# Kernel tuning notes

Hardware: AMD Instinct MI355X
Metric: run time of the kernel (lower is better)

Reference implementation:

```python
import jax, jax.numpy as jnp
import numpy as np

NUM_GROUPS = 32
EPS = 1e-6


def group_norm(x, w, b):
    # x: (B, C, L); normalize per group of C//32 channels over (channels-in-group, L)
    B, C, L = x.shape
    xg = x.reshape(B, NUM_GROUPS, C // NUM_GROUPS, L)
    mean = jnp.mean(xg, axis=(2, 3), keepdims=True)
    var = jnp.var(xg, axis=(2, 3), keepdims=True)
    xn = ((xg - mean) * jax.lax.rsqrt(var + EPS)).reshape(B, C, L)
    return xn * w[None, :, None] + b[None, :, None]


def conv1x1(x, w, b):
    # 1x1 Conv1d == channel-mixing linear. x: (B,C,L), w: (O,C), b: (O,)
    return jnp.einsum('oc,bcl->bol', w, x) + b[None, :, None]


def setup_inputs() -> dict:
    key = jax.random.key(0)
    ks = jax.random.split(key, 6)
    B, C, L = 8, 512, 2048
    s = 1.0 / np.sqrt(C)
    return {
        'x': jax.random.normal(ks[0], (B, C, L), dtype=jnp.float32),
        'gn_w': jnp.ones((C,), jnp.float32),
        'gn_b': jnp.zeros((C,), jnp.float32),
        'wq': jax.random.normal(ks[1], (C, C), dtype=jnp.float32) * s,
        'bq': jnp.zeros((C,), jnp.float32),
        'wk': jax.random.normal(ks[2], (C, C), dtype=jnp.float32) * s,
        'bk': jnp.zeros((C,), jnp.float32),
        'wv': jax.random.normal(ks[3], (C, C), dtype=jnp.float32) * s,
        'bv': jnp.zeros((C,), jnp.float32),
        'wo': jax.random.normal(ks[4], (C, C), dtype=jnp.float32) * s,
        'bo': jnp.zeros((C,), jnp.float32),
    }


def reference(x, gn_w, gn_b, wq, bq, wk, bk, wv, bv, wo, bo):
    B, C, L = x.shape
    h = group_norm(x, gn_w, gn_b)
    q = conv1x1(h, wq, bq)  # (B,C,L)
    k = conv1x1(h, wk, bk)
    v = conv1x1(h, wv, bv)
    scale = jnp.asarray(C, x.dtype) ** -0.5
    # scores over length: w[b,i,j] = sum_c q[b,c,i] k[b,c,j]
    w_ = jnp.einsum('bci,bcj->bij', q, k) * scale
    w_ = jax.nn.softmax(w_, axis=-1)
    # h[b,c,i] = sum_j w[b,i,j] v[b,c,j]
    h = jnp.einsum('bij,bcj->bci', w_, v)
    h = conv1x1(h, wo, bo)
    return x + h
```

## Files before the change

### kernel.cpp

```cpp
#include <hip/hip_runtime.h>
#include <math.h>

#define BATCH 8
#define CH 512
#define LEN 2048
#define NG 32
#define CPG 16

typedef unsigned short u16;
typedef __bf16 bf16x8 __attribute__((ext_vector_type(8)));
typedef float f32x16 __attribute__((ext_vector_type(16)));

__device__ __forceinline__ u16 f2bf(float f) {
    union { float f; unsigned u; } c; c.f = f;
    unsigned r = c.u + 0x7fffu + ((c.u >> 16) & 1u);
    return (u16)(r >> 16);
}
__device__ __forceinline__ float bf2f(u16 h) {
    union { unsigned u; float f; } c; c.u = ((unsigned)h) << 16;
    return c.f;
}
__device__ __forceinline__ void gload16(const u16* g, u16* l) {
    __builtin_amdgcn_global_load_lds(
        (const __attribute__((address_space(1))) unsigned int*)g,
        (__attribute__((address_space(3))) unsigned int*)l, 16, 0, 0);
}

__global__ __launch_bounds__(256) void fused_pre(
    const float* __restrict__ x,
    const float* __restrict__ w0, const float* __restrict__ w1,
    const float* __restrict__ w2, const float* __restrict__ w3,
    u16* __restrict__ o0, u16* __restrict__ o1,
    u16* __restrict__ o2, u16* __restrict__ o3,
    float4* __restrict__ zbuf, float* __restrict__ stats) {
    const int blk = blockIdx.x;
    if (blk < 16) {
        zbuf[blk * 256 + threadIdx.x] = make_float4(0.f, 0.f, 0.f, 0.f);
    } else if (blk < 1040) {
        const int wb = blk - 16;
        const float* s; u16* d;
        switch (wb >> 8) {
            case 0: s = w0; d = o0; break;
            case 1: s = w1; d = o1; break;
            case 2: s = w2; d = o2; break;
            default: s = w3; d = o3; break;
        }
        const int i = (wb & 255) * 256 + threadIdx.x;
        float4 f = ((const float4*)s)[i];
        ((ushort4*)d)[i] = make_ushort4(f2bf(f.x), f2bf(f.y), f2bf(f.z), f2bf(f.w));
    } else {
        const int sb = blk - 1040;
        const int b = sb >> 7, g = (sb >> 2) & 31, sl = sb & 3;
        const float4* xp = (const float4*)(x + ((size_t)b * CH + (size_t)g * CPG) * LEN) + sl * 2048;
        float s = 0.f, s2 = 0.f;
        #pragma unroll
        for (int i = 0; i < 8; ++i) {
            float4 v = xp[threadIdx.x + i * 256];
            s += v.x + v.y + v.z + v.w;
            s2 = fmaf(v.x, v.x, fmaf(v.y, v.y, fmaf(v.z, v.z, fmaf(v.w, v.w, s2))));
        }
        #pragma unroll
        for (int off = 32; off > 0; off >>= 1) {
            s  += __shfl_down(s, off, 64);
            s2 += __shfl_down(s2, off, 64);
        }
        __shared__ float sm[2][4];
        const int lane = threadIdx.x & 63, wv = threadIdx.x >> 6;
        if (lane == 0) { sm[0][wv] = s; sm[1][wv] = s2; }
        __syncthreads();
        if (threadIdx.x == 0) {
            const int base = (b * NG + g) * 4 + sl;
            stats[base]        = sm[0][0] + sm[0][1] + sm[0][2] + sm[0][3];
            stats[1024 + base] = sm[1][0] + sm[1][1] + sm[1][2] + sm[1][3];
        }
    }
}

__global__ __launch_bounds__(256) void gn_apply_t(const float* __restrict__ x,
                                                  const float* __restrict__ stats,
                                                  const float* __restrict__ gw,
                                                  const float* __restrict__ gb,
                                                  u16* __restrict__ Ht) {
    __shared__ float tile[64][65];
    const int b = blockIdx.z, c0 = blockIdx.y * 64, l0 = blockIdx.x * 64;
    const int t = threadIdx.x;
    const int rid = t >> 4, q = t & 15;
    const float inv = 1.f / (CPG * LEN);
    #pragma unroll
    for (int pass = 0; pass < 4; ++pass) {
        const int c = rid + pass * 16;
        const int ca = c0 + c;
        const int base = (b * NG + (ca >> 4)) * 4;
        const float S  = stats[base + 0] + stats[base + 1] + stats[base + 2] + stats[base + 3];
        const float S2 = stats[1024 + base + 0] + stats[1024 + base + 1]
                       + stats[1024 + base + 2] + stats[1024 + base + 3];
        const float mean = S * inv;
        const float var  = S2 * inv - mean * mean;
        const float a  = rsqrtf(var + 1e-6f) * gw[ca];
        const float sh = gb[ca] - mean * a;
        const float4 v = *(const float4*)&x[((size_t)b * CH + ca) * LEN + l0 + q * 4];
        tile[c][q * 4 + 0] = v.x * a + sh;
        tile[c][q * 4 + 1] = v.y * a + sh;
        tile[c][q * 4 + 2] = v.z * a + sh;
        tile[c][q * 4 + 3] = v.w * a + sh;
    }
    __syncthreads();
    #pragma unroll
    for (int pass = 0; pass < 4; ++pass) {
        const int l = rid + pass * 16;
        ushort4 o;
        o.x = f2bf(tile[q * 4 + 0][l]);
        o.y = f2bf(tile[q * 4 + 1][l]);
        o.z = f2bf(tile[q * 4 + 2][l]);
        o.w = f2bf(tile[q * 4 + 3][l]);
        *(ushort4*)&Ht[((size_t)b * LEN + l0 + l) * CH + c0 + q * 4] = o;
    }
}

#define EPI_QK   0
#define EPI_TBN  1
#define EPI_EXP  2
#define EPI_TNRM 3
#define EPI_FIN  4

template <int MODE>
__global__ __launch_bounds__(256, 4) void gemm_bt(
    const u16* __restrict__ A, int lda, long long sA,
    const u16* __restrict__ B, int ldb, long long sB,
    void* __restrict__ Out, void* __restrict__ Out2,
    int ldo, long long sO,
    const float* __restrict__ bias, const float* __restrict__ bias2,
    const float* __restrict__ res, long long sR,
    float* __restrict__ rsum, long long sRS,
    int K, float alpha) {
    __shared__ u16 As[128 * 64];
    __shared__ u16 Bs[128 * 64];

    int bz, by, bx;
    if (MODE == EPI_EXP) {
        const int gx = gridDim.x, gy = gridDim.y;
        int flat = (blockIdx.z * gy + blockIdx.y) * gx + blockIdx.x;
        const int nbk = gx * gy * (int)gridDim.z;
        flat = (flat & 7) * (nbk >> 3) + (flat >> 3);
        bz = flat / (gx * gy);
        const int rr = flat - bz * gx * gy;
        by = rr / gx;
        bx = rr - by * gx;
    } else {
        bz = blockIdx.z; by = blockIdx.y; bx = blockIdx.x;
    }

    const int n0 = bx * 128, m0 = by * 128;
    A += (size_t)bz * sA;
    B += (size_t)bz * sB;
    const int t = threadIdx.x;
    const int lane = t & 63, wid = t >> 6;

    const int rowL = t >> 3, kq = (t & 7) ^ (rowL & 7);
    unsigned aoff = (unsigned)((m0 + rowL) * lda + kq * 8);
    unsigned boff = (unsigned)((n0 + rowL) * ldb + kq * 8);
    u16* const lds_dst_a = As + t * 8;
    u16* const lds_dst_b = Bs + t * 8;

    f32x16 acc[2][2];
    #pragma unroll
    for (int i = 0; i < 2; ++i)
        #pragma unroll
        for (int j = 0; j < 2; ++j)
            acc[i][j] = (f32x16)(0.f);

    const int col = lane & 31, half = lane >> 5;
    const int wm = (wid & 1) * 64, wn = (wid >> 1) * 64;
    const int mf = wm + col, nf = wn + col;
    const int mswz = mf & 7, nswz = nf & 7;

    for (int k0 = 0; k0 < K; k0 += 64) {
        #pragma unroll
        for (int g = 0; g < 4; ++g) {
            gload16(A + aoff + g * (32 * lda), lds_dst_a + g * 2048);
            gload16(B + boff + g * (32 * ldb), lds_dst_b + g * 2048);
        }
        aoff += 64; boff += 64;
        __syncthreads();
        #pragma unroll
        for (int ks = 0; ks < 4; ++ks) {
            const int kcA = ((ks * 2 + half) ^ mswz) * 8;
            const int kcB = ((ks * 2 + half) ^ nswz) * 8;
            bf16x8 a0 = *(const bf16x8*)(As + (mf)      * 64 + kcA);
            bf16x8 a1 = *(const bf16x8*)(As + (mf + 32) * 64 + kcA);
            bf16x8 b0 = *(const bf16x8*)(Bs + (nf)      * 64 + kcB);
            bf16x8 b1 = *(const bf16x8*)(Bs + (nf + 32) * 64 + kcB);
            acc[0][0] = __builtin_amdgcn_mfma_f32_32x32x16_bf16(a0, b0, acc[0][0], 0, 0, 0);
            acc[0][1] = __builtin_amdgcn_mfma_f32_32x32x16_bf16(a0, b1, acc[0][1], 0, 0, 0);
            acc[1][0] = __builtin_amdgcn_mfma_f32_32x32x16_bf16(a1, b0, acc[1][0], 0, 0, 0);
            acc[1][1] = __builtin_amdgcn_mfma_f32_32x32x16_bf16(a1, b1, acc[1][1], 0, 0, 0);
        }
        __syncthreads();
    }

    if (MODE == EPI_FIN) {
        float* O = (float*)Out + (size_t)bz * sO;
        const float* R = res + (size_t)bz * sR;
        #pragma unroll
        for (int im = 0; im < 2; ++im)
            #pragma unroll
            for (int g4 = 0; g4 < 4; ++g4) {
                const int mb = m0 + wm + im * 32 + g4 * 8 + half * 4;
                #pragma unroll
                for (int jn = 0; jn < 2; ++jn) {
                    const int n = n0 + wn + jn * 32 + col;
                    const float bb = bias[n];
                    const size_t base = (size_t)n * ldo + mb;
                    const float4 r4 = *(const float4*)&R[base];
                    float4 o4;
                    o4.x = acc[im][jn][g4 * 4 + 0] + bb + r4.x;
                    o4.y = acc[im][jn][g4 * 4 + 1] + bb + r4.y;
                    o4.z = acc[im][jn][g4 * 4 + 2] + bb + r4.z;
                    o4.w = acc[im][jn][g4 * 4 + 3] + bb + r4.w;
                    *(float4*)&O[base] = o4;
                }
            }
    } else if (MODE == EPI_EXP) {
        u16* O = (u16*)Out + (size_t)bz * sO;
        float* RS = rsum + (size_t)bz * sRS;
        float psum[2] = {0.f, 0.f};
        #pragma unroll
        for (int im = 0; im < 2; ++im)
            #pragma unroll
            for (int g4 = 0; g4 < 4; ++g4) {
                const int mb = m0 + wm + im * 32 + g4 * 8 + half * 4;
                #pragma unroll
                for (int jn = 0; jn < 2; ++jn) {
                    const int n = n0 + wn + jn * 32 + col;
                    u16 h0 = f2bf(__expf(acc[im][jn][g4 * 4 + 0] * alpha));
                    u16 h1 = f2bf(__expf(acc[im][jn][g4 * 4 + 1] * alpha));
                    u16 h2 = f2bf(__expf(acc[im][jn][g4 * 4 + 2] * alpha));
                    u16 h3 = f2bf(__expf(acc[im][jn][g4 * 4 + 3] * alpha));
                    psum[jn] += bf2f(h0) + bf2f(h1) + bf2f(h2) + bf2f(h3);
                    *(ushort4*)&O[(size_t)n * ldo + mb] = make_ushort4(h0, h1, h2, h3);
                }
            }
        #pragma unroll
        for (int jn = 0; jn < 2; ++jn) psum[jn] += __shfl_xor(psum[jn], 32, 64);
        if (half == 0) {
            #pragma unroll
            for (int jn = 0; jn < 2; ++jn)
                atomicAdd(&RS[n0 + wn + jn * 32 + col], psum[jn]);
        }
    } else {
        u16* O;
        const float* bi = bias;
        const float* RS = (MODE == EPI_TNRM) ? rsum + (size_t)bz * sRS : nullptr;
        int mbase = m0 + wm;
        if (MODE == EPI_QK) {
            const bool hi = (m0 & 512) != 0;
            O  = (u16*)(hi ? Out2 : Out) + (size_t)bz * sO;
            bi = hi ? bias2 : bias;
            mbase = (m0 & 511) + wm;
        } else {
            O = (u16*)Out + (size_t)bz * sO;
        }
        float inv[2];
        if (MODE == EPI_TNRM) {
            inv[0] = 1.f / RS[n0 + wn + col];
            inv[1] = 1.f / RS[n0 + wn + 32 + col];
        }
        #pragma unroll
        for (int im = 0; im < 2; ++im)
            #pragma unroll
            for (int g4 = 0; g4 < 4; ++g4) {
                const int mb = mbase + im * 32 + g4 * 8 + half * 4;
                float4 bm = make_float4(0.f, 0.f, 0.f, 0.f);
                if (MODE == EPI_QK) bm = *(const float4*)&bi[mb];
                #pragma unroll
                for (int jn = 0; jn < 2; ++jn) {
                    const int n = n0 + wn + jn * 32 + col;
                    float v0 = acc[im][jn][g4 * 4 + 0];
                    float v1 = acc[im][jn][g4 * 4 + 1];
                    float v2 = acc[im][jn][g4 * 4 + 2];
                    float v3 = acc[im][jn][g4 * 4 + 3];
                    if (MODE == EPI_QK)  { v0 += bm.x; v1 += bm.y; v2 += bm.z; v3 += bm.w; }
                    if (MODE == EPI_TBN) { const float bb = bi[n]; v0 += bb; v1 += bb; v2 += bb; v3 += bb; }
                    if (MODE == EPI_TNRM) { v0 *= inv[jn]; v1 *= inv[jn]; v2 *= inv[jn]; v3 *= inv[jn]; }
                    ushort4 pk = make_ushort4(f2bf(v0), f2bf(v1), f2bf(v2), f2bf(v3));
                    *(ushort4*)&O[(size_t)n * ldo + mb] = pk;
                }
            }
    }
}

extern "C" void kernel_launch(void* const* d_in, const int* in_sizes, int n_in,
                              void* d_out, int out_size, void* d_ws, size_t ws_size,
                              hipStream_t stream) {
    const float* x    = (const float*)d_in[0];
    const float* gn_w = (const float*)d_in[1];
    const float* gn_b = (const float*)d_in[2];
    const float* wq   = (const float*)d_in[3];
    const float* bq   = (const float*)d_in[4];
    const float* wk   = (const float*)d_in[5];
    const float* bk   = (const float*)d_in[6];
    const float* wv   = (const float*)d_in[7];
    const float* bv   = (const float*)d_in[8];
    const float* wo   = (const float*)d_in[9];
    const float* bo   = (const float*)d_in[10];
    float* out = (float*)d_out;

    char* p = (char*)d_ws;
    const size_t WSZ = (size_t)CH * CH * 2;
    const size_t HSZ = (size_t)BATCH * CH * LEN * 2;
    u16* Wqk = (u16*)p; p += 2 * WSZ;
    u16* Wvb = (u16*)p; p += WSZ;
    u16* Wob = (u16*)p; p += WSZ;
    u16* Ht  = (u16*)p; p += HSZ;
    u16* Qt  = (u16*)p; p += HSZ;
    u16* Kt  = (u16*)p; p += HSZ;
    u16* Vb  = (u16*)p; p += HSZ;
    u16* Sb  = (u16*)p; p += (size_t)BATCH * LEN * LEN * 2;
    float* rowsum = (float*)p; p += (size_t)BATCH * LEN * 4;
    float* stats  = (float*)p;

    const long long sH = (long long)LEN * CH;
    const long long sV = (long long)CH * LEN;
    const long long sS = (long long)LEN * LEN;
    const float scale = 0.04419417382415922f;

    fused_pre<<<2064, 256, 0, stream>>>(x, wq, wk, wv, wo,
                                        Wqk, Wqk + (size_t)CH * CH, Wvb, Wob,
                                        (float4*)rowsum, stats);
    gn_apply_t<<<dim3(LEN / 64, CH / 64, BATCH), 256, 0, stream>>>(x, stats, gn_w, gn_b, Ht);

    gemm_bt<EPI_QK><<<dim3(16, 8, 8), 256, 0, stream>>>(
        Wqk, CH, 0, Ht, CH, sH, Qt, Kt, CH, sH, bq, bk, nullptr, 0, nullptr, 0, CH, 0.f);
    gemm_bt<EPI_TBN><<<dim3(4, 16, 8), 256, 0, stream>>>(
        Ht, CH, sH, Wvb, CH, 0, Vb, nullptr, LEN, sV, bv, nullptr, nullptr, 0, nullptr, 0, CH, 0.f);
    gemm_bt<EPI_EXP><<<dim3(16, 16, 8), 256, 0, stream>>>(
        Kt, CH, sH, Qt, CH, sH, Sb, nullptr, LEN, sS, nullptr, nullptr, nullptr, 0, rowsum, LEN, CH, scale);
    gemm_bt<EPI_TNRM><<<dim3(16, 4, 8), 256, 0, stream>>>(
        Vb, LEN, sV, Sb, LEN, sS, Ht, nullptr, CH, sH, nullptr, nullptr, nullptr, 0, rowsum, LEN, LEN, 0.f);
    gemm_bt<EPI_FIN><<<dim3(4, 16, 8), 256, 0, stream>>>(
        Ht, CH, sH, Wob, CH, 0, out, nullptr, LEN, sV, bo, nullptr, x, sV, nullptr, 0, CH, 0.f);
}
```

Measured before the change: 271.4 us.

## Merge V projection and exp-score GEMMs into one heterogeneous launch

Replaces the separate V-projection GEMM launch and the QK^T exp-score GEMM launch with a single kernel whose grid covers both. The first 2048 blocks compute the scores (keeping the XCD-aware block remap) and the remaining 512 compute V with its bias. This removes one launch and the tail or idle gap between the two GEMMs, letting the small V GEMM fill leftover slots. The risk is that the branch adds code size or register pressure, and the V blocks run last as a tail.

```diff
diff --git a/kernel.cpp b/kernel.cpp
--- a/kernel.cpp
+++ b/kernel.cpp
@@ -118,8 +118,6 @@
 }
 
 #define EPI_QK   0
-#define EPI_TBN  1
-#define EPI_EXP  2
 #define EPI_TNRM 3
 #define EPI_FIN  4
 
@@ -136,20 +134,7 @@
     __shared__ u16 As[128 * 64];
     __shared__ u16 Bs[128 * 64];
 
-    int bz, by, bx;
-    if (MODE == EPI_EXP) {
-        const int gx = gridDim.x, gy = gridDim.y;
-        int flat = (blockIdx.z * gy + blockIdx.y) * gx + blockIdx.x;
-        const int nbk = gx * gy * (int)gridDim.z;
-        flat = (flat & 7) * (nbk >> 3) + (flat >> 3);
-        bz = flat / (gx * gy);
-        const int rr = flat - bz * gx * gy;
-        by = rr / gx;
-        bx = rr - by * gx;
-    } else {
-        bz = blockIdx.z; by = blockIdx.y; bx = blockIdx.x;
-    }
-
+    const int bz = blockIdx.z, by = blockIdx.y, bx = blockIdx.x;
     const int n0 = bx * 128, m0 = by * 128;
     A += (size_t)bz * sA;
     B += (size_t)bz * sB;
@@ -220,33 +205,6 @@
                     *(float4*)&O[base] = o4;
                 }
             }
-    } else if (MODE == EPI_EXP) {
-        u16* O = (u16*)Out + (size_t)bz * sO;
-        float* RS = rsum + (size_t)bz * sRS;
-        float psum[2] = {0.f, 0.f};
-        #pragma unroll
-        for (int im = 0; im < 2; ++im)
-            #pragma unroll
-            for (int g4 = 0; g4 < 4; ++g4) {
-                const int mb = m0 + wm + im * 32 + g4 * 8 + half * 4;
-                #pragma unroll
-                for (int jn = 0; jn < 2; ++jn) {
-                    const int n = n0 + wn + jn * 32 + col;
-                    u16 h0 = f2bf(__expf(acc[im][jn][g4 * 4 + 0] * alpha));
-                    u16 h1 = f2bf(__expf(acc[im][jn][g4 * 4 + 1] * alpha));
-                    u16 h2 = f2bf(__expf(acc[im][jn][g4 * 4 + 2] * alpha));
-                    u16 h3 = f2bf(__expf(acc[im][jn][g4 * 4 + 3] * alpha));
-                    psum[jn] += bf2f(h0) + bf2f(h1) + bf2f(h2) + bf2f(h3);
-                    *(ushort4*)&O[(size_t)n * ldo + mb] = make_ushort4(h0, h1, h2, h3);
-                }
-            }
-        #pragma unroll
-        for (int jn = 0; jn < 2; ++jn) psum[jn] += __shfl_xor(psum[jn], 32, 64);
-        if (half == 0) {
-            #pragma unroll
-            for (int jn = 0; jn < 2; ++jn)
-                atomicAdd(&RS[n0 + wn + jn * 32 + col], psum[jn]);
-        }
     } else {
         u16* O;
         const float* bi = bias;
@@ -280,10 +238,134 @@
                     float v2 = acc[im][jn][g4 * 4 + 2];
                     float v3 = acc[im][jn][g4 * 4 + 3];
                     if (MODE == EPI_QK)  { v0 += bm.x; v1 += bm.y; v2 += bm.z; v3 += bm.w; }
-                    if (MODE == EPI_TBN) { const float bb = bi[n]; v0 += bb; v1 += bb; v2 += bb; v3 += bb; }
                     if (MODE == EPI_TNRM) { v0 *= inv[jn]; v1 *= inv[jn]; v2 *= inv[jn]; v3 *= inv[jn]; }
                     ushort4 pk = make_ushort4(f2bf(v0), f2bf(v1), f2bf(v2), f2bf(v3));
                     *(ushort4*)&O[(size_t)n * ldo + mb] = pk;
+                }
+            }
+    }
+}
+
+__global__ __launch_bounds__(256, 4) void gemm_sv(
+    const u16* __restrict__ Kt, const u16* __restrict__ Qt,
+    const u16* __restrict__ Ht, const u16* __restrict__ Wvb,
+    u16* __restrict__ Sb, u16* __restrict__ Vb,
+    const float* __restrict__ bv, float* __restrict__ rowsum,
+    float alpha) {
+    __shared__ u16 As[128 * 64];
+    __shared__ u16 Bs[128 * 64];
+
+    const long long sH = (long long)LEN * CH;
+    const int blk = blockIdx.x;
+    const bool isV = blk >= 2048;
+    int bz, by, bx;
+    const u16 *A, *B;
+    u16* O;
+    if (!isV) {
+        int flat = (blk & 7) * 256 + (blk >> 3);
+        bz = flat >> 8;
+        const int rr = flat & 255;
+        by = rr >> 4; bx = rr & 15;
+        A = Kt + (size_t)bz * sH;
+        B = Qt + (size_t)bz * sH;
+        O = Sb + (size_t)bz * ((long long)LEN * LEN);
+    } else {
+        const int v = blk - 2048;
+        bz = v >> 6;
+        const int rr = v & 63;
+        by = rr >> 2; bx = rr & 3;
+        A = Ht + (size_t)bz * sH;
+        B = Wvb;
+        O = Vb + (size_t)bz * ((long long)CH * LEN);
+    }
+
+    const int n0 = bx * 128, m0 = by * 128;
+    const int t = threadIdx.x;
+    const int lane = t & 63, wid = t >> 6;
+
+    const int rowL = t >> 3, kq = (t & 7) ^ (rowL & 7);
+    unsigned aoff = (unsigned)((m0 + rowL) * CH + kq * 8);
+    unsigned boff = (unsigned)((n0 + rowL) * CH + kq * 8);
+    u16* const lds_dst_a = As + t * 8;
+    u16* const lds_dst_b = Bs + t * 8;
+
+    f32x16 acc[2][2];
+    #pragma unroll
+    for (int i = 0; i < 2; ++i)
+        #pragma unroll
+        for (int j = 0; j < 2; ++j)
+            acc[i][j] = (f32x16)(0.f);
+
+    const int col = lane & 31, half = lane >> 5;
+    const int wm = (wid & 1) * 64, wn = (wid >> 1) * 64;
+    const int mf = wm + col, nf = wn + col;
+    const int mswz = mf & 7, nswz = nf & 7;
+
+    for (int k0 = 0; k0 < CH; k0 += 64) {
+        #pragma unroll
+        for (int g = 0; g < 4; ++g) {
+            gload16(A + aoff + g * (32 * CH), lds_dst_a + g * 2048);
+            gload16(B + boff + g * (32 * CH), lds_dst_b + g * 2048);
+        }
+        aoff += 64; boff += 64;
+        __syncthreads();
+        #pragma unroll
+        for (int ks = 0; ks < 4; ++ks) {
+            const int kcA = ((ks * 2 + half) ^ mswz) * 8;
+            const int kcB = ((ks * 2 + half) ^ nswz) * 8;
+            bf16x8 a0 = *(const bf16x8*)(As + (mf)      * 64 + kcA);
+            bf16x8 a1 = *(const bf16x8*)(As + (mf + 32) * 64 + kcA);
+            bf16x8 b0 = *(const bf16x8*)(Bs + (nf)      * 64 + kcB);
+            bf16x8 b1 = *(const bf16x8*)(Bs + (nf + 32) * 64 + kcB);
+            acc[0][0] = __builtin_amdgcn_mfma_f32_32x32x16_bf16(a0, b0, acc[0][0], 0, 0, 0);
+            acc[0][1] = __builtin_amdgcn_mfma_f32_32x32x16_bf16(a0, b1, acc[0][1], 0, 0, 0);
+            acc[1][0] = __builtin_amdgcn_mfma_f32_32x32x16_bf16(a1, b0, acc[1][0], 0, 0, 0);
+            acc[1][1] = __builtin_amdgcn_mfma_f32_32x32x16_bf16(a1, b1, acc[1][1], 0, 0, 0);
+        }
+        __syncthreads();
+    }
+
+    if (!isV) {
+        float* RS = rowsum + (size_t)bz * LEN;
+        float psum[2] = {0.f, 0.f};
+        #pragma unroll
+        for (int im = 0; im < 2; ++im)
+            #pragma unroll
+            for (int g4 = 0; g4 < 4; ++g4) {
+                const int mb = m0 + wm + im * 32 + g4 * 8 + half * 4;
+                #pragma unroll
+                for (int jn = 0; jn < 2; ++jn) {
+                    const int n = n0 + wn + jn * 32 + col;
+                    u16 h0 = f2bf(__expf(acc[im][jn][g4 * 4 + 0] * alpha));
+                    u16 h1 = f2bf(__expf(acc[im][jn][g4 * 4 + 1] * alpha));
+                    u16 h2 = f2bf(__expf(acc[im][jn][g4 * 4 + 2] * alpha));
+                    u16 h3 = f2bf(__expf(acc[im][jn][g4 * 4 + 3] * alpha));
+                    psum[jn] += bf2f(h0) + bf2f(h1) + bf2f(h2) + bf2f(h3);
+                    *(ushort4*)&O[(size_t)n * LEN + mb] = make_ushort4(h0, h1, h2, h3);
+                }
+            }
+        #pragma unroll
+        for (int jn = 0; jn < 2; ++jn) psum[jn] += __shfl_xor(psum[jn], 32, 64);
+        if (half == 0) {
+            #pragma unroll
+            for (int jn = 0; jn < 2; ++jn)
+                atomicAdd(&RS[n0 + wn + jn * 32 + col], psum[jn]);
+        }
+    } else {
+        #pragma unroll
+        for (int im = 0; im < 2; ++im)
+            #pragma unroll
+            for (int g4 = 0; g4 < 4; ++g4) {
+                const int mb = m0 + wm + im * 32 + g4 * 8 + half * 4;
+                #pragma unroll
+                for (int jn = 0; jn < 2; ++jn) {
+                    const int n = n0 + wn + jn * 32 + col;
+                    const float bb = bv[n];
+                    ushort4 pk = make_ushort4(f2bf(acc[im][jn][g4 * 4 + 0] + bb),
+                                              f2bf(acc[im][jn][g4 * 4 + 1] + bb),
+                                              f2bf(acc[im][jn][g4 * 4 + 2] + bb),
+                                              f2bf(acc[im][jn][g4 * 4 + 3] + bb));
+                    *(ushort4*)&O[(size_t)n * LEN + mb] = pk;
                 }
             }
     }
@@ -321,7 +403,6 @@
 
     const long long sH = (long long)LEN * CH;
     const long long sV = (long long)CH * LEN;
-    const long long sS = (long long)LEN * LEN;
     const float scale = 0.04419417382415922f;
 
     fused_pre<<<2064, 256, 0, stream>>>(x, wq, wk, wv, wo,
@@ -331,12 +412,10 @@
 
     gemm_bt<EPI_QK><<<dim3(16, 8, 8), 256, 0, stream>>>(
         Wqk, CH, 0, Ht, CH, sH, Qt, Kt, CH, sH, bq, bk, nullptr, 0, nullptr, 0, CH, 0.f);
-    gemm_bt<EPI_TBN><<<dim3(4, 16, 8), 256, 0, stream>>>(
-        Ht, CH, sH, Wvb, CH, 0, Vb, nullptr, LEN, sV, bv, nullptr, nullptr, 0, nullptr, 0, CH, 0.f);
-    gemm_bt<EPI_EXP><<<dim3(16, 16, 8), 256, 0, stream>>>(
-        Kt, CH, sH, Qt, CH, sH, Sb, nullptr, LEN, sS, nullptr, nullptr, nullptr, 0, rowsum, LEN, CH, scale);
+    gemm_sv<<<2560, 256, 0, stream>>>(Kt, Qt, Ht, Wvb, Sb, Vb, bv, rowsum, scale);
     gemm_bt<EPI_TNRM><<<dim3(16, 4, 8), 256, 0, stream>>>(
-        Vb, LEN, sV, Sb, LEN, sS, Ht, nullptr, CH, sH, nullptr, nullptr, nullptr, 0, rowsum, LEN, LEN, 0.f);
+        Vb, LEN, sV, Sb, LEN, (long long)LEN * LEN, Ht, nullptr, CH, sH,
+        nullptr, nullptr, nullptr, 0, rowsum, LEN, LEN, 0.f);
     gemm_bt<EPI_FIN><<<dim3(4, 16, 8), 256, 0, stream>>>(
         Ht, CH, sH, Wob, CH, 0, out, nullptr, LEN, sV, bo, nullptr, x, sV, nullptr, 0, CH, 0.f);
 }
```

Result: faster. 265.8 us (-2.1%).
